# Kernel tuning notes

Hardware: AMD Instinct MI355X
Metric: run time of the kernel (lower is better)

## Reference

```python
import jax, jax.numpy as jnp
import numpy as np
from jax import lax

N_NODES = 10000
N_EDGES = 160000
F_NODE = 128
C_GCN = 64
S_SEQ = 32
T_SEQ = 96
H_LSTM = 128


def setup_inputs() -> dict:
    key = jax.random.key(0)
    ks = jax.random.split(key, 20)
    inp = {
        "sequences": jax.random.normal(ks[0], (N_NODES, T_SEQ, S_SEQ), jnp.float32),
        "edge_index": jax.random.randint(ks[1], (2, N_EDGES), 0, N_NODES, jnp.int64),
        "edge_attr": jax.random.uniform(ks[2], (N_EDGES, 1), jnp.float32),
        "node_features": jax.random.normal(ks[3], (N_NODES, F_NODE), jnp.float32),
        "node_indices": jax.random.randint(ks[4], (N_NODES,), 0, N_NODES, jnp.int64),
    }
    s_g = 1.0 / np.sqrt(F_NODE)
    inp["gcn_w"] = jax.random.uniform(ks[5], (F_NODE, C_GCN), jnp.float32, -s_g, s_g)
    inp["gcn_b"] = jnp.zeros((C_GCN,), jnp.float32)
    in0 = S_SEQ + C_GCN
    s_l = 1.0 / np.sqrt(H_LSTM)
    inp["w_ih0"] = jax.random.uniform(ks[6], (4 * H_LSTM, in0), jnp.float32, -s_l, s_l)
    inp["w_hh0"] = jax.random.uniform(ks[7], (4 * H_LSTM, H_LSTM), jnp.float32, -s_l, s_l)
    inp["b_ih0"] = jax.random.uniform(ks[8], (4 * H_LSTM,), jnp.float32, -s_l, s_l)
    inp["b_hh0"] = jax.random.uniform(ks[9], (4 * H_LSTM,), jnp.float32, -s_l, s_l)
    inp["w_ih1"] = jax.random.uniform(ks[10], (4 * H_LSTM, H_LSTM), jnp.float32, -s_l, s_l)
    inp["w_hh1"] = jax.random.uniform(ks[11], (4 * H_LSTM, H_LSTM), jnp.float32, -s_l, s_l)
    inp["b_ih1"] = jax.random.uniform(ks[12], (4 * H_LSTM,), jnp.float32, -s_l, s_l)
    inp["b_hh1"] = jax.random.uniform(ks[13], (4 * H_LSTM,), jnp.float32, -s_l, s_l)
    s_f = 1.0 / np.sqrt(H_LSTM)
    inp["fc_w"] = jax.random.uniform(ks[14], (1, H_LSTM), jnp.float32, -s_f, s_f)
    inp["fc_b"] = jnp.zeros((1,), jnp.float32)
    return inp


def gcn_conv(x, edge_index, w, b):
    """PyG GCNConv: out = D^{-1/2} (A + I) D^{-1/2} X W + b."""
    n = x.shape[0]
    xw = x @ w  # [N, C]
    loop = jnp.arange(n, dtype=edge_index.dtype)
    row = jnp.concatenate([edge_index[0], loop])  # source j
    col = jnp.concatenate([edge_index[1], loop])  # target i
    deg = jax.ops.segment_sum(jnp.ones_like(col, dtype=xw.dtype), col, num_segments=n)
    dinv = jnp.where(deg > 0, lax.rsqrt(deg), 0.0)
    norm = dinv[row] * dinv[col]  # [E+N]
    msg = xw[row] * norm[:, None]  # gather + scale
    out = jax.ops.segment_sum(msg, col, num_segments=n)  # scatter-add
    return out + b


def lstm_layer(x, w_ih, w_hh, b_ih, b_hh):
    """batch_first LSTM layer; torch gate order i,f,g,o. x: [N,T,I] -> [N,T,H]."""
    n, t, _ = x.shape
    h_dim = w_hh.shape[1]
    xg = jnp.einsum("nti,gi->ntg", x, w_ih) + b_ih + b_hh  # [N,T,4H]

    def step(carry, xt):
        h, c = carry
        g = xt + h @ w_hh.T
        i, f, gg, o = jnp.split(g, 4, axis=-1)
        c = jax.nn.sigmoid(f) * c + jax.nn.sigmoid(i) * jnp.tanh(gg)
        h = jax.nn.sigmoid(o) * jnp.tanh(c)
        return (h, c), h

    h0 = jnp.zeros((n, h_dim), x.dtype)
    _, hs = lax.scan(step, (h0, h0), jnp.swapaxes(xg, 0, 1))
    return jnp.swapaxes(hs, 0, 1)


def reference(sequences, edge_index, edge_attr, node_features, node_indices,
              gcn_w, gcn_b, w_ih0, w_hh0, b_ih0, b_hh0,
              w_ih1, w_hh1, b_ih1, b_hh1, fc_w, fc_b):
    # GCN over the static graph (dropout = identity in eval mode)
    gcn_out = gcn_conv(node_features, edge_index, gcn_w, gcn_b)  # [N, C]
    t = sequences.shape[1]
    gcn_rep = jnp.broadcast_to(gcn_out[:, None, :], (gcn_out.shape[0], t, gcn_out.shape[1]))
    combined = jnp.concatenate([sequences, gcn_rep], axis=-1)  # [N, T, S+C]
    h = lstm_layer(combined, w_ih0, w_hh0, b_ih0, b_hh0)
    h = lstm_layer(h, w_ih1, w_hh1, b_ih1, b_hh1)
    last = h[:, -1, :]  # [N, H]
    return last @ fc_w.T + fc_b  # [N, 1]
```

## Files before the change

### kernel.cpp

```cpp
#include <hip/hip_runtime.h>
#include <hip/hip_bf16.h>

typedef _Float16 half8 __attribute__((ext_vector_type(8)));
typedef float floatx4 __attribute__((ext_vector_type(4)));
typedef float floatx2 __attribute__((ext_vector_type(2)));

#define N_NODES 10000
#define F_NODE  128
#define C_GCN   64
#define N_EDGES 160000
#define T_SEQ   96
#define S_SEQ   32
#define HID     128
#define M_BLK   40
#define MT      3
#define SEQ_STRIDE 104
#define H_STRIDE   136
#define WAVE_STREAM 61440

__device__ __forceinline__ float fast_rcp(float x) { return __builtin_amdgcn_rcpf(x); }
__device__ __forceinline__ float sigm_f(float x) {
    return fast_rcp(1.0f + __expf(-x));
}
__device__ __forceinline__ float tanh_f(float x) {
    return 2.0f * fast_rcp(1.0f + __expf(-2.0f * x)) - 1.0f;
}

__global__ void k_gcn_xw(const float* __restrict__ nf, const float* __restrict__ w,
                         float* __restrict__ xw) {
    int tid = blockIdx.x * 256 + threadIdx.x;
    int n = tid >> 6, c = tid & 63;
    if (n >= N_NODES) return;
    float s = 0.f;
    #pragma unroll 8
    for (int k = 0; k < F_NODE; ++k) s = fmaf(nf[n * F_NODE + k], w[k * C_GCN + c], s);
    xw[n * C_GCN + c] = s;
}

__global__ void k_deg_init(float* __restrict__ deg) {
    int i = blockIdx.x * 256 + threadIdx.x;
    if (i < N_NODES) deg[i] = 1.0f;
}

__global__ void k_deg_count(const int* __restrict__ ei, float* __restrict__ deg) {
    int e = blockIdx.x * 256 + threadIdx.x;
    if (e < N_EDGES) atomicAdd(&deg[ei[N_EDGES + e]], 1.0f);
}

__global__ void k_dinv(const float* __restrict__ deg, float* __restrict__ dinv) {
    int i = blockIdx.x * 256 + threadIdx.x;
    if (i < N_NODES) dinv[i] = rsqrtf(deg[i]);
}

__global__ void k_gcn_self(const float* __restrict__ xw, const float* __restrict__ dinv,
                           const float* __restrict__ gb, float* __restrict__ gout) {
    int tid = blockIdx.x * 256 + threadIdx.x;
    int n = tid >> 6, c = tid & 63;
    if (n >= N_NODES) return;
    float di = dinv[n];
    gout[tid] = xw[tid] * di * di + gb[c];
}

__global__ void k_gcn_scatter(const int* __restrict__ ei, const float* __restrict__ xw,
                              const float* __restrict__ dinv, float* __restrict__ gout) {
    int e = blockIdx.x * 4 + (threadIdx.x >> 6);
    int c = threadIdx.x & 63;
    if (e >= N_EDGES) return;
    int r  = ei[e];
    int cl = ei[N_EDGES + e];
    float nm = dinv[r] * dinv[cl];
    atomicAdd(&gout[cl * C_GCN + c], xw[r * C_GCN + c] * nm);
}

__global__ void k_pack(const float* __restrict__ w_ih0, const float* __restrict__ w_hh0,
                       const float* __restrict__ w_ih1, const float* __restrict__ w_hh1,
                       half8* __restrict__ pP) {
    int tid = blockIdx.x * 256 + threadIdx.x;
    if (tid >= 8 * 15 * 4 * 64) return;
    int lane = tid & 63;
    int g    = (tid >> 6) & 3;
    int s    = (tid >> 8) % 15;
    int w    = tid / 3840;
    const float* src; int kt, K;
    if (s < 3)       { src = w_ih0; kt = s;      K = 96;  }
    else if (s < 7)  { src = w_hh0; kt = s - 3;  K = 128; }
    else if (s < 11) { src = w_ih1; kt = s - 7;  K = 128; }
    else             { src = w_hh1; kt = s - 11; K = 128; }
    int row = g * 128 + w * 16 + (lane & 15);
    int k0  = kt * 32 + (lane >> 4) * 8;
    half8 v;
    #pragma unroll
    for (int j = 0; j < 8; ++j) v[j] = (_Float16)src[row * K + k0 + j];
    pP[tid] = v;
}

__global__ void k_bsum(const float* __restrict__ bi0, const float* __restrict__ bh0,
                       const float* __restrict__ bi1, const float* __restrict__ bh1,
                       float* __restrict__ bs) {
    int i = blockIdx.x * 256 + threadIdx.x;
    if (i < 512)       bs[i] = bi0[i] + bh0[i];
    else if (i < 1024) bs[i] = bi1[i - 512] + bh1[i - 512];
}


__device__ __forceinline__ void async_copy16(const void* g, void* l) {
    __builtin_amdgcn_global_load_lds(
        (const __attribute__((address_space(1))) unsigned int*)g,
        (__attribute__((address_space(3))) unsigned int*)l, 16, 0, 0);
}

__device__ __forceinline__ void dma_slot(const char* __restrict__ src, int lane, _Float16* slot) {
    #pragma unroll
    for (int g = 0; g < 4; ++g)
        async_copy16((const void*)(src + g * 1024 + lane * 16), (void*)(slot + g * 512));
}

#define VMW(N) asm volatile("s_waitcnt vmcnt(" #N ")" ::: "memory")

#define BARRIER_NOVM() do {                                   \
    asm volatile("s_waitcnt lgkmcnt(0)" ::: "memory");        \
    __builtin_amdgcn_s_barrier();                             \
    asm volatile("" ::: "memory");                            \
} while (0)

#define RDB(BG, BUF) {                                                      \
    _Pragma("unroll")                                                       \
    for (int g = 0; g < 4; ++g) (BG)[g] = *(const half8*)((BUF) + g * 512 + lane * 8); }

#define RDA(AA, APTR, KOFF, ASTR) {                                         \
    _Pragma("unroll")                                                       \
    for (int mt = 0; mt < MT; ++mt)                                         \
        (AA)[mt] = *(const half8*)((APTR) + (mt * 16 + l15) * (ASTR) + (KOFF) + quad * 8); }

#define MM(AA, BG) {                                                        \
    _Pragma("unroll")                                                       \
    for (int g = 0; g < 4; ++g)                                             \
        _Pragma("unroll")                                                   \
        for (int mt = 0; mt < MT; ++mt)                                     \
            acc[g][mt] = __builtin_amdgcn_mfma_f32_16x16x32_f16((AA)[mt], (BG)[g], acc[g][mt], 0, 0, 0); }

#define ACCINIT(B) {                                                        \
    _Pragma("unroll")                                                       \
    for (int g = 0; g < 4; ++g) {                                           \
        floatx4 bv = {(B)[g], (B)[g], (B)[g], (B)[g]};                      \
        _Pragma("unroll")                                                   \
        for (int mt = 0; mt < MT; ++mt) acc[g][mt] = bv;                    \
    } }

__device__ __forceinline__ void epilogue(floatx4 acc[4][MT],
                                         float c[MT][4], _Float16* Hnext,
                                         int quad, int ch) {
    #pragma unroll
    for (int mt = 0; mt < MT; ++mt) {
        #pragma unroll
        for (int r = 0; r < 4; ++r) {
            float gi = acc[0][mt][r];
            float gf = acc[1][mt][r];
            float gg = acc[2][mt][r];
            float go = acc[3][mt][r];
            float cn = sigm_f(gf) * c[mt][r] + sigm_f(gi) * tanh_f(gg);
            c[mt][r] = cn;
            float h = sigm_f(go) * tanh_f(cn);
            Hnext[(mt * 16 + quad * 4 + r) * H_STRIDE + ch] = (_Float16)h;
        }
    }
}

__global__ __launch_bounds__(512, 2) void k_lstm(
    const float* __restrict__ seq, const float* __restrict__ gcn,
    const char* __restrict__ pW, const float* __restrict__ bsum,
    const float* __restrict__ fcw, const float* __restrict__ fcb,
    float* __restrict__ out) {

    __shared__ __align__(16) _Float16 sSeq[48 * SEQ_STRIDE];
    __shared__ __align__(16) _Float16 sH0[2][48 * H_STRIDE];
    __shared__ __align__(16) _Float16 sH1[2][48 * H_STRIDE];
    __shared__ __align__(16) _Float16 sWa[8][2048];
    __shared__ __align__(16) _Float16 sWb[8][2048];
    __shared__ __align__(16) _Float16 sWc[8][2048];

    const int tid  = threadIdx.x;
    const int wid  = tid >> 6;
    const int lane = tid & 63;
    const int l15  = lane & 15;
    const int quad = lane >> 4;
    const int node0 = blockIdx.x * M_BLK;
    const int ch = wid * 16 + l15;
    const bool rot = (wid >= 4);

    _Float16* const rb0 = &sWa[wid][0];
    _Float16* const rb1 = &sWb[wid][0];
    _Float16* const rb2 = &sWc[wid][0];

    const char* pWw = pW + wid * WAVE_STREAM;

#define DMA(S, RB) dma_slot(pWw + (S) * 4096, lane, (RB))

    if (!rot) { DMA(0, rb0); DMA(1, rb1); }
    else      { DMA(3, rb0); DMA(4, rb1); }

    for (int i = tid; i < 48 * SEQ_STRIDE; i += 512) sSeq[i] = (_Float16)0.f;
    for (int i = tid; i < 48 * H_STRIDE; i += 512) {
        sH0[0][i] = (_Float16)0.f; sH0[1][i] = (_Float16)0.f;
        sH1[0][i] = (_Float16)0.f; sH1[1][i] = (_Float16)0.f;
    }

    float bias0[4], bias1[4];
    #pragma unroll
    for (int g = 0; g < 4; ++g) {
        bias0[g] = bsum[g * 128 + ch];
        bias1[g] = bsum[512 + g * 128 + ch];
    }

    float c0[MT][4] = {{0}}, c1[MT][4] = {{0}};

    __syncthreads();

    for (int i = tid; i < M_BLK * (C_GCN / 2); i += 512) {
        int r = i >> 5, cp = (i & 31) * 2;
        floatx2 v = *(const floatx2*)(gcn + (size_t)(node0 + r) * C_GCN + cp);
        sSeq[r * SEQ_STRIDE + S_SEQ + cp]     = (_Float16)v.x;
        sSeq[r * SEQ_STRIDE + S_SEQ + cp + 1] = (_Float16)v.y;
    }
    {
        int r = tid >> 4, cp = (tid & 15) * 2;
        if (tid < M_BLK * 16) {
            floatx2 v = *(const floatx2*)(seq + ((size_t)(node0 + r) * T_SEQ) * S_SEQ + cp);
            sSeq[r * SEQ_STRIDE + cp]     = (_Float16)v.x;
            sSeq[r * SEQ_STRIDE + cp + 1] = (_Float16)v.y;
        }
    }
    __syncthreads();

    floatx4 acc[4][MT];
    half8 aX[MT], aY[MT], bX[4], bY[4];

    RDB(bX, rb0);

    const int pr = tid >> 4, pc = (tid & 15) * 2;
    const int r1 = 32 + ((tid & 127) >> 4);
    floatx2 pfa, pfb;

    if (!rot) {
      for (int t = 0; t < T_SEQ; ++t) {
        const int cur = t & 1, nxt = cur ^ 1;
        const _Float16* h0c = &sH0[cur][0];
        _Float16*       h0n = &sH0[nxt][0];
        const _Float16* h1c = &sH1[cur][0];
        _Float16*       h1n = &sH1[nxt][0];
        {
            int tp = (t + 1 < T_SEQ) ? (t + 1) : (T_SEQ - 1);
            pfa = *(const floatx2*)(seq + ((size_t)(node0 + pr) * T_SEQ + tp) * S_SEQ + pc);
            pfb = *(const floatx2*)(seq + ((size_t)(node0 + r1) * T_SEQ + tp) * S_SEQ + pc);
        }
        ACCINIT(bias0);
        RDA(aX, sSeq, 0, SEQ_STRIDE);
        DMA(2, rb2);  VMW(6); RDB(bY, rb1); RDA(aY, sSeq, 32, SEQ_STRIDE); MM(aX, bX);
        DMA(3, rb0);  VMW(4); RDB(bX, rb2); RDA(aX, sSeq, 64, SEQ_STRIDE); MM(aY, bY);
        DMA(4, rb1);  VMW(4); RDB(bY, rb0); RDA(aY, h0c, 0,  H_STRIDE);    MM(aX, bX);
        DMA(5, rb2);  VMW(4); RDB(bX, rb1); RDA(aX, h0c, 32, H_STRIDE);    MM(aY, bY);
        DMA(6, rb0);  VMW(4); RDB(bY, rb2); RDA(aY, h0c, 64, H_STRIDE);    MM(aX, bX);
        DMA(7, rb1);  VMW(4); RDB(bX, rb0); RDA(aX, h0c, 96, H_STRIDE);    MM(aY, bY);
        DMA(8, rb2);  VMW(4); RDB(bY, rb1);                                MM(aX, bX);
        epilogue(acc, c0, h0n, quad, ch);
        BARRIER_NOVM();
        ACCINIT(bias1);
        RDA(aY, h0n, 0, H_STRIDE);
        DMA(9,  rb0); VMW(4); RDB(bX, rb2); RDA(aX, h0n, 32, H_STRIDE); MM(aY, bY);
        DMA(10, rb1); VMW(4); RDB(bY, rb0); RDA(aY, h0n, 64, H_STRIDE); MM(aX, bX);
        DMA(11, rb2); VMW(4); RDB(bX, rb1); RDA(aX, h0n, 96, H_STRIDE); MM(aY, bY);
        DMA(12, rb0); VMW(4); RDB(bY, rb2); RDA(aY, h1c, 0,  H_STRIDE); MM(aX, bX);
        DMA(13, rb1); VMW(4); RDB(bX, rb0); RDA(aX, h1c, 32, H_STRIDE); MM(aY, bY);
        DMA(14, rb2); VMW(4); RDB(bY, rb1); RDA(aY, h1c, 64, H_STRIDE); MM(aX, bX);
        DMA(0,  rb0); VMW(4); RDB(bX, rb2); RDA(aX, h1c, 96, H_STRIDE); MM(aY, bY);
        DMA(1,  rb1); VMW(4); MM(aX, bX);   RDB(bX, rb0);
        if (t + 1 < T_SEQ) {
            sSeq[pr * SEQ_STRIDE + pc]     = (_Float16)pfa.x;
            sSeq[pr * SEQ_STRIDE + pc + 1] = (_Float16)pfa.y;
            if (tid < 128) {
                sSeq[r1 * SEQ_STRIDE + pc]     = (_Float16)pfb.x;
                sSeq[r1 * SEQ_STRIDE + pc + 1] = (_Float16)pfb.y;
            }
        }
        epilogue(acc, c1, h1n, quad, ch);
        BARRIER_NOVM();
      }
    } else {
      for (int t = 0; t < T_SEQ; ++t) {
        const int cur = t & 1, nxt = cur ^ 1;
        const _Float16* h0c = &sH0[cur][0];
        _Float16*       h0n = &sH0[nxt][0];
        const _Float16* h1c = &sH1[cur][0];
        _Float16*       h1n = &sH1[nxt][0];
        {
            int tp = (t + 1 < T_SEQ) ? (t + 1) : (T_SEQ - 1);
            pfa = *(const floatx2*)(seq + ((size_t)(node0 + pr) * T_SEQ + tp) * S_SEQ + pc);
            pfb = *(const floatx2*)(seq + ((size_t)(node0 + r1) * T_SEQ + tp) * S_SEQ + pc);
        }
        ACCINIT(bias0);
        RDA(aX, h0c, 0, H_STRIDE);
        DMA(5,  rb2); VMW(6); RDB(bY, rb1); RDA(aY, h0c, 32, H_STRIDE);    MM(aX, bX);
        DMA(6,  rb0); VMW(4); RDB(bX, rb2); RDA(aX, h0c, 64, H_STRIDE);    MM(aY, bY);
        DMA(0,  rb1); VMW(4); RDB(bY, rb0); RDA(aY, h0c, 96, H_STRIDE);    MM(aX, bX);
        DMA(1,  rb2); VMW(4); RDB(bX, rb1); RDA(aX, sSeq, 0,  SEQ_STRIDE); MM(aY, bY);
        DMA(2,  rb0); VMW(4); RDB(bY, rb2); RDA(aY, sSeq, 32, SEQ_STRIDE); MM(aX, bX);
        DMA(11, rb1); VMW(4); RDB(bX, rb0); RDA(aX, sSeq, 64, SEQ_STRIDE); MM(aY, bY);
        DMA(12, rb2); VMW(4); RDB(bY, rb1);                                MM(aX, bX);
        epilogue(acc, c0, h0n, quad, ch);
        BARRIER_NOVM();
        ACCINIT(bias1);
        RDA(aY, h1c, 0, H_STRIDE);
        DMA(13, rb0); VMW(4); RDB(bX, rb2); RDA(aX, h1c, 32, H_STRIDE); MM(aY, bY);
        DMA(14, rb1); VMW(4); RDB(bY, rb0); RDA(aY, h1c, 64, H_STRIDE); MM(aX, bX);
        DMA(7,  rb2); VMW(4); RDB(bX, rb1); RDA(aX, h1c, 96, H_STRIDE); MM(aY, bY);
        DMA(8,  rb0); VMW(4); RDB(bY, rb2); RDA(aY, h0n, 0,  H_STRIDE); MM(aX, bX);
        DMA(9,  rb1); VMW(4); RDB(bX, rb0); RDA(aX, h0n, 32, H_STRIDE); MM(aY, bY);
        DMA(10, rb2); VMW(4); RDB(bY, rb1); RDA(aY, h0n, 64, H_STRIDE); MM(aX, bX);
        DMA(3,  rb0); VMW(4); RDB(bX, rb2); RDA(aX, h0n, 96, H_STRIDE); MM(aY, bY);
        DMA(4,  rb1); VMW(4); MM(aX, bX);   RDB(bX, rb0);
        if (t + 1 < T_SEQ) {
            sSeq[pr * SEQ_STRIDE + pc]     = (_Float16)pfa.x;
            sSeq[pr * SEQ_STRIDE + pc + 1] = (_Float16)pfa.y;
            if (tid < 128) {
                sSeq[r1 * SEQ_STRIDE + pc]     = (_Float16)pfb.x;
                sSeq[r1 * SEQ_STRIDE + pc + 1] = (_Float16)pfb.y;
            }
        }
        epilogue(acc, c1, h1n, quad, ch);
        BARRIER_NOVM();
      }
    }

#undef DMA

    asm volatile("s_waitcnt vmcnt(0)" ::: "memory");

    if (tid < M_BLK) {
        const _Float16* h1 = &sH1[0][tid * H_STRIDE];
        float s = fcb[0];
        #pragma unroll 16
        for (int k = 0; k < HID; ++k) s = fmaf((float)h1[k], fcw[k], s);
        out[node0 + tid] = s;
    }
}

extern "C" void kernel_launch(void* const* d_in, const int* in_sizes, int n_in,
                              void* d_out, int out_size, void* d_ws, size_t ws_size,
                              hipStream_t stream) {
    const float* seq   = (const float*)d_in[0];
    const int*   ei    = (const int*)d_in[1];
    const float* nf    = (const float*)d_in[3];
    const float* gcn_w = (const float*)d_in[5];
    const float* gcn_b = (const float*)d_in[6];
    const float* w_ih0 = (const float*)d_in[7];
    const float* w_hh0 = (const float*)d_in[8];
    const float* b_ih0 = (const float*)d_in[9];
    const float* b_hh0 = (const float*)d_in[10];
    const float* w_ih1 = (const float*)d_in[11];
    const float* w_hh1 = (const float*)d_in[12];
    const float* b_ih1 = (const float*)d_in[13];
    const float* b_hh1 = (const float*)d_in[14];
    const float* fc_w  = (const float*)d_in[15];
    const float* fc_b  = (const float*)d_in[16];
    float* out = (float*)d_out;

    char* ws = (char*)d_ws;
    float* xw   = (float*)(ws);
    float* gout = (float*)(ws + 2621440);
    float* deg  = (float*)(ws + 5242880);
    float* dinv = (float*)(ws + 5283840);
    float* bsum = (float*)(ws + 5324800);
    char*  pP   = (char*)(ws + 5328896);

    k_gcn_xw     <<<2500,  256, 0, stream>>>(nf, gcn_w, xw);
    k_deg_init   <<<40,    256, 0, stream>>>(deg);
    k_deg_count  <<<625,   256, 0, stream>>>(ei, deg);
    k_dinv       <<<40,    256, 0, stream>>>(deg, dinv);
    k_gcn_self   <<<2500,  256, 0, stream>>>(xw, dinv, gcn_b, gout);
    k_gcn_scatter<<<40000, 256, 0, stream>>>(ei, xw, dinv, gout);

    k_pack<<<120, 256, 0, stream>>>(w_ih0, w_hh0, w_ih1, w_hh1, (half8*)pP);
    k_bsum<<<4,   256, 0, stream>>>(b_ih0, b_hh0, b_ih1, b_hh1, bsum);

    k_lstm<<<250, 512, 0, stream>>>(seq, gout, pP, bsum, fc_w, fc_b, out);
}
```

Before: 1.161 ms.

## Keep six layer-0 weight k-tiles resident in registers, stream the rest

```diff
diff --git a/kernel.cpp b/kernel.cpp
--- a/kernel.cpp
+++ b/kernel.cpp
@@ -16,7 +16,9 @@
 #define MT      3
 #define SEQ_STRIDE 104
 #define H_STRIDE   136
-#define WAVE_STREAM 61440
+#define RES_SZ    196608
+#define RES_WAVE  24576
+#define STR_WAVE  36864
 
 __device__ __forceinline__ float fast_rcp(float x) { return __builtin_amdgcn_rcpf(x); }
 __device__ __forceinline__ float sigm_f(float x) {
@@ -74,24 +76,34 @@
 
 __global__ void k_pack(const float* __restrict__ w_ih0, const float* __restrict__ w_hh0,
                        const float* __restrict__ w_ih1, const float* __restrict__ w_hh1,
-                       half8* __restrict__ pP) {
+                       char* __restrict__ pP) {
     int tid = blockIdx.x * 256 + threadIdx.x;
-    if (tid >= 8 * 15 * 4 * 64) return;
+    if (tid >= 30720) return;
     int lane = tid & 63;
-    int g    = (tid >> 6) & 3;
-    int s    = (tid >> 8) % 15;
-    int w    = tid / 3840;
-    const float* src; int kt, K;
-    if (s < 3)       { src = w_ih0; kt = s;      K = 96;  }
-    else if (s < 7)  { src = w_hh0; kt = s - 3;  K = 128; }
-    else if (s < 11) { src = w_ih1; kt = s - 7;  K = 128; }
-    else             { src = w_hh1; kt = s - 11; K = 128; }
+    int rest = tid >> 6;
+    int w    = rest / 60;
+    int idx  = rest % 60;
+    const float* src; int K, kt, g;
+    size_t dst;
+    if (idx < 24) {
+        int i = idx >> 2; g = idx & 3;
+        int grp = i / 3; kt = i % 3;
+        src = grp ? w_hh0 : w_ih0; K = grp ? 128 : 96;
+        dst = (size_t)w * RES_WAVE + (size_t)idx * 1024 + lane * 16;
+    } else {
+        int j = idx - 24; int s = j >> 2; g = j & 3;
+        if (s == 0)      { src = w_hh0; kt = 3; }
+        else if (s <= 4) { src = w_ih1; kt = s - 1; }
+        else             { src = w_hh1; kt = s - 5; }
+        K = 128;
+        dst = (size_t)RES_SZ + (size_t)w * STR_WAVE + (size_t)s * 4096 + (size_t)g * 1024 + lane * 16;
+    }
     int row = g * 128 + w * 16 + (lane & 15);
     int k0  = kt * 32 + (lane >> 4) * 8;
     half8 v;
     #pragma unroll
     for (int j = 0; j < 8; ++j) v[j] = (_Float16)src[row * K + k0 + j];
-    pP[tid] = v;
+    *(half8*)(pP + dst) = v;
 }
 
 __global__ void k_bsum(const float* __restrict__ bi0, const float* __restrict__ bh0,
@@ -192,12 +204,19 @@
     _Float16* const rb1 = &sWb[wid][0];
     _Float16* const rb2 = &sWc[wid][0];
 
-    const char* pWw = pW + wid * WAVE_STREAM;
-
-#define DMA(S, RB) dma_slot(pWw + (S) * 4096, lane, (RB))
-
-    if (!rot) { DMA(0, rb0); DMA(1, rb1); }
-    else      { DMA(3, rb0); DMA(4, rb1); }
+    const char* pSw = pW + RES_SZ + (size_t)wid * STR_WAVE;
+
+#define DMA(S, RB) dma_slot(pSw + (S) * 4096, lane, (RB))
+
+    half8 rW[6][4];
+    {
+        const half8* pR = (const half8*)(pW + (size_t)wid * RES_WAVE);
+        #pragma unroll
+        for (int i = 0; i < 6; ++i)
+            #pragma unroll
+            for (int g = 0; g < 4; ++g)
+                rW[i][g] = pR[(i * 4 + g) * 64 + lane];
+    }
 
     for (int i = tid; i < 48 * SEQ_STRIDE; i += 512) sSeq[i] = (_Float16)0.f;
     for (int i = tid; i < 48 * H_STRIDE; i += 512) {
@@ -232,10 +251,11 @@
     }
     __syncthreads();
 
+    if (!rot) { DMA(0, rb0); DMA(1, rb1); DMA(2, rb2); }
+    else      { DMA(0, rb0); DMA(5, rb1); DMA(6, rb2); }
+
     floatx4 acc[4][MT];
     half8 aX[MT], aY[MT], bX[4], bY[4];
-
-    RDB(bX, rb0);
 
     const int pr = tid >> 4, pc = (tid & 15) * 2;
     const int r1 = 32 + ((tid & 127) >> 4);
@@ -255,25 +275,26 @@
         }
         ACCINIT(bias0);
         RDA(aX, sSeq, 0, SEQ_STRIDE);
-        DMA(2, rb2);  VMW(6); RDB(bY, rb1); RDA(aY, sSeq, 32, SEQ_STRIDE); MM(aX, bX);
-        DMA(3, rb0);  VMW(4); RDB(bX, rb2); RDA(aX, sSeq, 64, SEQ_STRIDE); MM(aY, bY);
-        DMA(4, rb1);  VMW(4); RDB(bY, rb0); RDA(aY, h0c, 0,  H_STRIDE);    MM(aX, bX);
-        DMA(5, rb2);  VMW(4); RDB(bX, rb1); RDA(aX, h0c, 32, H_STRIDE);    MM(aY, bY);
-        DMA(6, rb0);  VMW(4); RDB(bY, rb2); RDA(aY, h0c, 64, H_STRIDE);    MM(aX, bX);
-        DMA(7, rb1);  VMW(4); RDB(bX, rb0); RDA(aX, h0c, 96, H_STRIDE);    MM(aY, bY);
-        DMA(8, rb2);  VMW(4); RDB(bY, rb1);                                MM(aX, bX);
+        RDA(aY, sSeq, 32, SEQ_STRIDE);   MM(aX, rW[0]);
+        RDA(aX, sSeq, 64, SEQ_STRIDE);   MM(aY, rW[1]);
+        RDA(aY, h0c, 0,  H_STRIDE);      MM(aX, rW[2]);
+        RDA(aX, h0c, 32, H_STRIDE);      MM(aY, rW[3]);
+        RDA(aY, h0c, 64, H_STRIDE);      MM(aX, rW[4]);
+        VMW(8); RDB(bX, rb0);
+        RDA(aX, h0c, 96, H_STRIDE);      MM(aY, rW[5]);
+        MM(aX, bX);
         epilogue(acc, c0, h0n, quad, ch);
         BARRIER_NOVM();
         ACCINIT(bias1);
-        RDA(aY, h0n, 0, H_STRIDE);
-        DMA(9,  rb0); VMW(4); RDB(bX, rb2); RDA(aX, h0n, 32, H_STRIDE); MM(aY, bY);
-        DMA(10, rb1); VMW(4); RDB(bY, rb0); RDA(aY, h0n, 64, H_STRIDE); MM(aX, bX);
-        DMA(11, rb2); VMW(4); RDB(bX, rb1); RDA(aX, h0n, 96, H_STRIDE); MM(aY, bY);
-        DMA(12, rb0); VMW(4); RDB(bY, rb2); RDA(aY, h1c, 0,  H_STRIDE); MM(aX, bX);
-        DMA(13, rb1); VMW(4); RDB(bX, rb0); RDA(aX, h1c, 32, H_STRIDE); MM(aY, bY);
-        DMA(14, rb2); VMW(4); RDB(bY, rb1); RDA(aY, h1c, 64, H_STRIDE); MM(aX, bX);
-        DMA(0,  rb0); VMW(4); RDB(bX, rb2); RDA(aX, h1c, 96, H_STRIDE); MM(aY, bY);
-        DMA(1,  rb1); VMW(4); MM(aX, bX);   RDB(bX, rb0);
+        VMW(4); RDB(bY, rb1); RDA(aY, h0n, 0, H_STRIDE); DMA(3, rb0);
+        VMW(4); RDB(bX, rb2); RDA(aX, h0n, 32, H_STRIDE); MM(aY, bY); DMA(4, rb1);
+        VMW(4); RDB(bY, rb0); RDA(aY, h0n, 64, H_STRIDE); MM(aX, bX); DMA(5, rb2);
+        VMW(4); RDB(bX, rb1); RDA(aX, h0n, 96, H_STRIDE); MM(aY, bY); DMA(6, rb0);
+        VMW(4); RDB(bY, rb2); RDA(aY, h1c, 0,  H_STRIDE); MM(aX, bX); DMA(7, rb1);
+        VMW(4); RDB(bX, rb0); RDA(aX, h1c, 32, H_STRIDE); MM(aY, bY); DMA(8, rb2);
+        VMW(4); RDB(bY, rb1); RDA(aY, h1c, 64, H_STRIDE); MM(aX, bX); DMA(0, rb0);
+        VMW(4); RDB(bX, rb2); RDA(aX, h1c, 96, H_STRIDE); MM(aY, bY); DMA(1, rb1);
+        MM(aX, bX); DMA(2, rb2);
         if (t + 1 < T_SEQ) {
             sSeq[pr * SEQ_STRIDE + pc]     = (_Float16)pfa.x;
             sSeq[pr * SEQ_STRIDE + pc + 1] = (_Float16)pfa.y;
@@ -299,25 +320,26 @@
         }
         ACCINIT(bias0);
         RDA(aX, h0c, 0, H_STRIDE);
-        DMA(5,  rb2); VMW(6); RDB(bY, rb1); RDA(aY, h0c, 32, H_STRIDE);    MM(aX, bX);
-        DMA(6,  rb0); VMW(4); RDB(bX, rb2); RDA(aX, h0c, 64, H_STRIDE);    MM(aY, bY);
-        DMA(0,  rb1); VMW(4); RDB(bY, rb0); RDA(aY, h0c, 96, H_STRIDE);    MM(aX, bX);
-        DMA(1,  rb2); VMW(4); RDB(bX, rb1); RDA(aX, sSeq, 0,  SEQ_STRIDE); MM(aY, bY);
-        DMA(2,  rb0); VMW(4); RDB(bY, rb2); RDA(aY, sSeq, 32, SEQ_STRIDE); MM(aX, bX);
-        DMA(11, rb1); VMW(4); RDB(bX, rb0); RDA(aX, sSeq, 64, SEQ_STRIDE); MM(aY, bY);
-        DMA(12, rb2); VMW(4); RDB(bY, rb1);                                MM(aX, bX);
+        RDA(aY, h0c, 32, H_STRIDE);      MM(aX, rW[3]);
+        RDA(aX, h0c, 64, H_STRIDE);      MM(aY, rW[4]);
+        VMW(8); RDB(bX, rb0);
+        RDA(aY, h0c, 96, H_STRIDE);      MM(aX, rW[5]);
+        RDA(aX, sSeq, 0, SEQ_STRIDE);    MM(aY, bX);
+        RDA(aY, sSeq, 32, SEQ_STRIDE);   MM(aX, rW[0]);
+        RDA(aX, sSeq, 64, SEQ_STRIDE);   MM(aY, rW[1]);
+        MM(aX, rW[2]);
         epilogue(acc, c0, h0n, quad, ch);
         BARRIER_NOVM();
         ACCINIT(bias1);
-        RDA(aY, h1c, 0, H_STRIDE);
-        DMA(13, rb0); VMW(4); RDB(bX, rb2); RDA(aX, h1c, 32, H_STRIDE); MM(aY, bY);
-        DMA(14, rb1); VMW(4); RDB(bY, rb0); RDA(aY, h1c, 64, H_STRIDE); MM(aX, bX);
-        DMA(7,  rb2); VMW(4); RDB(bX, rb1); RDA(aX, h1c, 96, H_STRIDE); MM(aY, bY);
-        DMA(8,  rb0); VMW(4); RDB(bY, rb2); RDA(aY, h0n, 0,  H_STRIDE); MM(aX, bX);
-        DMA(9,  rb1); VMW(4); RDB(bX, rb0); RDA(aX, h0n, 32, H_STRIDE); MM(aY, bY);
-        DMA(10, rb2); VMW(4); RDB(bY, rb1); RDA(aY, h0n, 64, H_STRIDE); MM(aX, bX);
-        DMA(3,  rb0); VMW(4); RDB(bX, rb2); RDA(aX, h0n, 96, H_STRIDE); MM(aY, bY);
-        DMA(4,  rb1); VMW(4); MM(aX, bX);   RDB(bX, rb0);
+        VMW(4); RDB(bY, rb1); RDA(aY, h1c, 0, H_STRIDE); DMA(7, rb0);
+        VMW(4); RDB(bX, rb2); RDA(aX, h1c, 32, H_STRIDE); MM(aY, bY); DMA(8, rb1);
+        VMW(4); RDB(bY, rb0); RDA(aY, h1c, 64, H_STRIDE); MM(aX, bX); DMA(1, rb2);
+        VMW(4); RDB(bX, rb1); RDA(aX, h1c, 96, H_STRIDE); MM(aY, bY); DMA(2, rb0);
+        VMW(4); RDB(bY, rb2); RDA(aY, h0n, 0,  H_STRIDE); MM(aX, bX); DMA(3, rb1);
+        VMW(4); RDB(bX, rb0); RDA(aX, h0n, 32, H_STRIDE); MM(aY, bY); DMA(4, rb2);
+        VMW(4); RDB(bY, rb1); RDA(aY, h0n, 64, H_STRIDE); MM(aX, bX); DMA(0, rb0);
+        VMW(4); RDB(bX, rb2); RDA(aX, h0n, 96, H_STRIDE); MM(aY, bY); DMA(5, rb1);
+        MM(aX, bX); DMA(6, rb2);
         if (t + 1 < T_SEQ) {
             sSeq[pr * SEQ_STRIDE + pc]     = (_Float16)pfa.x;
             sSeq[pr * SEQ_STRIDE + pc + 1] = (_Float16)pfa.y;
@@ -379,7 +401,7 @@
     k_gcn_self   <<<2500,  256, 0, stream>>>(xw, dinv, gcn_b, gout);
     k_gcn_scatter<<<40000, 256, 0, stream>>>(ei, xw, dinv, gout);
 
-    k_pack<<<120, 256, 0, stream>>>(w_ih0, w_hh0, w_ih1, w_hh1, (half8*)pP);
+    k_pack<<<120, 256, 0, stream>>>(w_ih0, w_hh0, w_ih1, w_hh1, pP);
     k_bsum<<<4,   256, 0, stream>>>(b_ih0, b_hh0, b_ih1, b_hh1, bsum);
 
     k_lstm<<<250, 512, 0, stream>>>(seq, gout, pP, bsum, fc_w, fc_b, out);
```

Measured after the change: 1.967 ms. 1.69x slower.

## Defer layer-1 LSTM epilogue into next step's layer-0 MFMA sequence

Applied to the files above, without the earlier changes.

```diff
diff --git a/kernel.cpp b/kernel.cpp
--- a/kernel.cpp
+++ b/kernel.cpp
@@ -132,20 +132,42 @@
     for (int mt = 0; mt < MT; ++mt)                                         \
         (AA)[mt] = *(const half8*)((APTR) + (mt * 16 + l15) * (ASTR) + (KOFF) + quad * 8); }
 
-#define MM(AA, BG) {                                                        \
+#define MM(ACC, AA, BG) {                                                   \
     _Pragma("unroll")                                                       \
     for (int g = 0; g < 4; ++g)                                             \
         _Pragma("unroll")                                                   \
         for (int mt = 0; mt < MT; ++mt)                                     \
-            acc[g][mt] = __builtin_amdgcn_mfma_f32_16x16x32_f16((AA)[mt], (BG)[g], acc[g][mt], 0, 0, 0); }
-
-#define ACCINIT(B) {                                                        \
+            (ACC)[g][mt] = __builtin_amdgcn_mfma_f32_16x16x32_f16((AA)[mt], (BG)[g], (ACC)[g][mt], 0, 0, 0); }
+
+#define ACCINIT(ACC, B) {                                                   \
     _Pragma("unroll")                                                       \
     for (int g = 0; g < 4; ++g) {                                           \
         floatx4 bv = {(B)[g], (B)[g], (B)[g], (B)[g]};                      \
         _Pragma("unroll")                                                   \
-        for (int mt = 0; mt < MT; ++mt) acc[g][mt] = bv;                    \
+        for (int mt = 0; mt < MT; ++mt) (ACC)[g][mt] = bv;                  \
     } }
+
+#define EPIC(MT_) if (t) {                                                  \
+    _Pragma("unroll")                                                       \
+    for (int r = 0; r < 4; ++r) {                                           \
+        float gi = acc1[0][MT_][r];                                         \
+        float gf = acc1[1][MT_][r];                                         \
+        float gg = acc1[2][MT_][r];                                         \
+        float go = acc1[3][MT_][r];                                         \
+        float cn = sigm_f(gf) * c1[MT_][r] + sigm_f(gi) * tanh_f(gg);       \
+        c1[MT_][r] = cn;                                                    \
+        h1b[(MT_ * 16 + quad * 4 + r) * H_STRIDE + ch] = (_Float16)(sigm_f(go) * tanh_f(cn)); } }
+
+#define EPICT(MT_) {                                                        \
+    _Pragma("unroll")                                                       \
+    for (int r = 0; r < 4; ++r) {                                           \
+        float gi = acc1[0][MT_][r];                                         \
+        float gf = acc1[1][MT_][r];                                         \
+        float gg = acc1[2][MT_][r];                                         \
+        float go = acc1[3][MT_][r];                                         \
+        float cn = sigm_f(gf) * c1[MT_][r] + sigm_f(gi) * tanh_f(gg);       \
+        c1[MT_][r] = cn;                                                    \
+        h1b[(MT_ * 16 + quad * 4 + r) * H_STRIDE + ch] = (_Float16)(sigm_f(go) * tanh_f(cn)); } }
 
 __device__ __forceinline__ void epilogue(floatx4 acc[4][MT],
                                          float c[MT][4], _Float16* Hnext,
@@ -174,7 +196,7 @@
 
     __shared__ __align__(16) _Float16 sSeq[48 * SEQ_STRIDE];
     __shared__ __align__(16) _Float16 sH0[2][48 * H_STRIDE];
-    __shared__ __align__(16) _Float16 sH1[2][48 * H_STRIDE];
+    __shared__ __align__(16) _Float16 sH1[48 * H_STRIDE];
     __shared__ __align__(16) _Float16 sWa[8][2048];
     __shared__ __align__(16) _Float16 sWb[8][2048];
     __shared__ __align__(16) _Float16 sWc[8][2048];
@@ -191,6 +213,7 @@
     _Float16* const rb0 = &sWa[wid][0];
     _Float16* const rb1 = &sWb[wid][0];
     _Float16* const rb2 = &sWc[wid][0];
+    _Float16* const h1b = &sH1[0];
 
     const char* pWw = pW + wid * WAVE_STREAM;
 
@@ -202,7 +225,7 @@
     for (int i = tid; i < 48 * SEQ_STRIDE; i += 512) sSeq[i] = (_Float16)0.f;
     for (int i = tid; i < 48 * H_STRIDE; i += 512) {
         sH0[0][i] = (_Float16)0.f; sH0[1][i] = (_Float16)0.f;
-        sH1[0][i] = (_Float16)0.f; sH1[1][i] = (_Float16)0.f;
+        sH1[i] = (_Float16)0.f;
     }
 
     float bias0[4], bias1[4];
@@ -232,7 +255,7 @@
     }
     __syncthreads();
 
-    floatx4 acc[4][MT];
+    floatx4 acc0[4][MT], acc1[4][MT];
     half8 aX[MT], aY[MT], bX[4], bY[4];
 
     RDB(bX, rb0);
@@ -246,34 +269,32 @@
         const int cur = t & 1, nxt = cur ^ 1;
         const _Float16* h0c = &sH0[cur][0];
         _Float16*       h0n = &sH0[nxt][0];
-        const _Float16* h1c = &sH1[cur][0];
-        _Float16*       h1n = &sH1[nxt][0];
         {
             int tp = (t + 1 < T_SEQ) ? (t + 1) : (T_SEQ - 1);
             pfa = *(const floatx2*)(seq + ((size_t)(node0 + pr) * T_SEQ + tp) * S_SEQ + pc);
             pfb = *(const floatx2*)(seq + ((size_t)(node0 + r1) * T_SEQ + tp) * S_SEQ + pc);
         }
-        ACCINIT(bias0);
+        ACCINIT(acc0, bias0);
         RDA(aX, sSeq, 0, SEQ_STRIDE);
-        DMA(2, rb2);  VMW(6); RDB(bY, rb1); RDA(aY, sSeq, 32, SEQ_STRIDE); MM(aX, bX);
-        DMA(3, rb0);  VMW(4); RDB(bX, rb2); RDA(aX, sSeq, 64, SEQ_STRIDE); MM(aY, bY);
-        DMA(4, rb1);  VMW(4); RDB(bY, rb0); RDA(aY, h0c, 0,  H_STRIDE);    MM(aX, bX);
-        DMA(5, rb2);  VMW(4); RDB(bX, rb1); RDA(aX, h0c, 32, H_STRIDE);    MM(aY, bY);
-        DMA(6, rb0);  VMW(4); RDB(bY, rb2); RDA(aY, h0c, 64, H_STRIDE);    MM(aX, bX);
-        DMA(7, rb1);  VMW(4); RDB(bX, rb0); RDA(aX, h0c, 96, H_STRIDE);    MM(aY, bY);
-        DMA(8, rb2);  VMW(4); RDB(bY, rb1);                                MM(aX, bX);
-        epilogue(acc, c0, h0n, quad, ch);
+        DMA(2, rb2);  VMW(6); RDB(bY, rb1); RDA(aY, sSeq, 32, SEQ_STRIDE); MM(acc0, aX, bX);
+        DMA(3, rb0);  VMW(4); RDB(bX, rb2); RDA(aX, sSeq, 64, SEQ_STRIDE); MM(acc0, aY, bY); EPIC(0);
+        DMA(4, rb1);  VMW(4); RDB(bY, rb0); RDA(aY, h0c, 0,  H_STRIDE);    MM(acc0, aX, bX);
+        DMA(5, rb2);  VMW(4); RDB(bX, rb1); RDA(aX, h0c, 32, H_STRIDE);    MM(acc0, aY, bY); EPIC(1);
+        DMA(6, rb0);  VMW(4); RDB(bY, rb2); RDA(aY, h0c, 64, H_STRIDE);    MM(acc0, aX, bX);
+        DMA(7, rb1);  VMW(4); RDB(bX, rb0); RDA(aX, h0c, 96, H_STRIDE);    MM(acc0, aY, bY); EPIC(2);
+        DMA(8, rb2);  VMW(4); RDB(bY, rb1);                                MM(acc0, aX, bX);
+        epilogue(acc0, c0, h0n, quad, ch);
         BARRIER_NOVM();
-        ACCINIT(bias1);
+        ACCINIT(acc1, bias1);
         RDA(aY, h0n, 0, H_STRIDE);
-        DMA(9,  rb0); VMW(4); RDB(bX, rb2); RDA(aX, h0n, 32, H_STRIDE); MM(aY, bY);
-        DMA(10, rb1); VMW(4); RDB(bY, rb0); RDA(aY, h0n, 64, H_STRIDE); MM(aX, bX);
-        DMA(11, rb2); VMW(4); RDB(bX, rb1); RDA(aX, h0n, 96, H_STRIDE); MM(aY, bY);
-        DMA(12, rb0); VMW(4); RDB(bY, rb2); RDA(aY, h1c, 0,  H_STRIDE); MM(aX, bX);
-        DMA(13, rb1); VMW(4); RDB(bX, rb0); RDA(aX, h1c, 32, H_STRIDE); MM(aY, bY);
-        DMA(14, rb2); VMW(4); RDB(bY, rb1); RDA(aY, h1c, 64, H_STRIDE); MM(aX, bX);
-        DMA(0,  rb0); VMW(4); RDB(bX, rb2); RDA(aX, h1c, 96, H_STRIDE); MM(aY, bY);
-        DMA(1,  rb1); VMW(4); MM(aX, bX);   RDB(bX, rb0);
+        DMA(9,  rb0); VMW(4); RDB(bX, rb2); RDA(aX, h0n, 32, H_STRIDE); MM(acc1, aY, bY);
+        DMA(10, rb1); VMW(4); RDB(bY, rb0); RDA(aY, h0n, 64, H_STRIDE); MM(acc1, aX, bX);
+        DMA(11, rb2); VMW(4); RDB(bX, rb1); RDA(aX, h0n, 96, H_STRIDE); MM(acc1, aY, bY);
+        DMA(12, rb0); VMW(4); RDB(bY, rb2); RDA(aY, h1b, 0,  H_STRIDE); MM(acc1, aX, bX);
+        DMA(13, rb1); VMW(4); RDB(bX, rb0); RDA(aX, h1b, 32, H_STRIDE); MM(acc1, aY, bY);
+        DMA(14, rb2); VMW(4); RDB(bY, rb1); RDA(aY, h1b, 64, H_STRIDE); MM(acc1, aX, bX);
+        DMA(0,  rb0); VMW(4); RDB(bX, rb2); RDA(aX, h1b, 96, H_STRIDE); MM(acc1, aY, bY);
+        DMA(1,  rb1); VMW(4); MM(acc1, aX, bX);   RDB(bX, rb0);
         if (t + 1 < T_SEQ) {
             sSeq[pr * SEQ_STRIDE + pc]     = (_Float16)pfa.x;
             sSeq[pr * SEQ_STRIDE + pc + 1] = (_Float16)pfa.y;
@@ -282,7 +303,6 @@
                 sSeq[r1 * SEQ_STRIDE + pc + 1] = (_Float16)pfb.y;
             }
         }
-        epilogue(acc, c1, h1n, quad, ch);
         BARRIER_NOVM();
       }
     } else {
@@ -290,34 +310,32 @@
         const int cur = t & 1, nxt = cur ^ 1;
         const _Float16* h0c = &sH0[cur][0];
         _Float16*       h0n = &sH0[nxt][0];
-        const _Float16* h1c = &sH1[cur][0];
-        _Float16*       h1n = &sH1[nxt][0];
         {
             int tp = (t + 1 < T_SEQ) ? (t + 1) : (T_SEQ - 1);
             pfa = *(const floatx2*)(seq + ((size_t)(node0 + pr) * T_SEQ + tp) * S_SEQ + pc);
             pfb = *(const floatx2*)(seq + ((size_t)(node0 + r1) * T_SEQ + tp) * S_SEQ + pc);
         }
-        ACCINIT(bias0);
+        ACCINIT(acc0, bias0);
         RDA(aX, h0c, 0, H_STRIDE);
-        DMA(5,  rb2); VMW(6); RDB(bY, rb1); RDA(aY, h0c, 32, H_STRIDE);    MM(aX, bX);
-        DMA(6,  rb0); VMW(4); RDB(bX, rb2); RDA(aX, h0c, 64, H_STRIDE);    MM(aY, bY);
-        DMA(0,  rb1); VMW(4); RDB(bY, rb0); RDA(aY, h0c, 96, H_STRIDE);    MM(aX, bX);
-        DMA(1,  rb2); VMW(4); RDB(bX, rb1); RDA(aX, sSeq, 0,  SEQ_STRIDE); MM(aY, bY);
-        DMA(2,  rb0); VMW(4); RDB(bY, rb2); RDA(aY, sSeq, 32, SEQ_STRIDE); MM(aX, bX);
-        DMA(11, rb1); VMW(4); RDB(bX, rb0); RDA(aX, sSeq, 64, SEQ_STRIDE); MM(aY, bY);
-        DMA(12, rb2); VMW(4); RDB(bY, rb1);                                MM(aX, bX);
-        epilogue(acc, c0, h0n, quad, ch);
+        DMA(5,  rb2); VMW(6); RDB(bY, rb1); RDA(aY, h0c, 32, H_STRIDE);    MM(acc0, aX, bX);
+        DMA(6,  rb0); VMW(4); RDB(bX, rb2); RDA(aX, h0c, 64, H_STRIDE);    MM(acc0, aY, bY); EPIC(0);
+        DMA(0,  rb1); VMW(4); RDB(bY, rb0); RDA(aY, h0c, 96, H_STRIDE);    MM(acc0, aX, bX);
+        DMA(1,  rb2); VMW(4); RDB(bX, rb1); RDA(aX, sSeq, 0,  SEQ_STRIDE); MM(acc0, aY, bY); EPIC(1);
+        DMA(2,  rb0); VMW(4); RDB(bY, rb2); RDA(aY, sSeq, 32, SEQ_STRIDE); MM(acc0, aX, bX);
+        DMA(11, rb1); VMW(4); RDB(bX, rb0); RDA(aX, sSeq, 64, SEQ_STRIDE); MM(acc0, aY, bY); EPIC(2);
+        DMA(12, rb2); VMW(4); RDB(bY, rb1);                                MM(acc0, aX, bX);
+        epilogue(acc0, c0, h0n, quad, ch);
         BARRIER_NOVM();
-        ACCINIT(bias1);
-        RDA(aY, h1c, 0, H_STRIDE);
-        DMA(13, rb0); VMW(4); RDB(bX, rb2); RDA(aX, h1c, 32, H_STRIDE); MM(aY, bY);
-        DMA(14, rb1); VMW(4); RDB(bY, rb0); RDA(aY, h1c, 64, H_STRIDE); MM(aX, bX);
-        DMA(7,  rb2); VMW(4); RDB(bX, rb1); RDA(aX, h1c, 96, H_STRIDE); MM(aY, bY);
-        DMA(8,  rb0); VMW(4); RDB(bY, rb2); RDA(aY, h0n, 0,  H_STRIDE); MM(aX, bX);
-        DMA(9,  rb1); VMW(4); RDB(bX, rb0); RDA(aX, h0n, 32, H_STRIDE); MM(aY, bY);
-        DMA(10, rb2); VMW(4); RDB(bY, rb1); RDA(aY, h0n, 64, H_STRIDE); MM(aX, bX);
-        DMA(3,  rb0); VMW(4); RDB(bX, rb2); RDA(aX, h0n, 96, H_STRIDE); MM(aY, bY);
-        DMA(4,  rb1); VMW(4); MM(aX, bX);   RDB(bX, rb0);
+        ACCINIT(acc1, bias1);
+        RDA(aY, h1b, 0, H_STRIDE);
+        DMA(13, rb0); VMW(4); RDB(bX, rb2); RDA(aX, h1b, 32, H_STRIDE); MM(acc1, aY, bY);
+        DMA(14, rb1); VMW(4); RDB(bY, rb0); RDA(aY, h1b, 64, H_STRIDE); MM(acc1, aX, bX);
+        DMA(7,  rb2); VMW(4); RDB(bX, rb1); RDA(aX, h1b, 96, H_STRIDE); MM(acc1, aY, bY);
+        DMA(8,  rb0); VMW(4); RDB(bY, rb2); RDA(aY, h0n, 0,  H_STRIDE); MM(acc1, aX, bX);
+        DMA(9,  rb1); VMW(4); RDB(bX, rb0); RDA(aX, h0n, 32, H_STRIDE); MM(acc1, aY, bY);
+        DMA(10, rb2); VMW(4); RDB(bY, rb1); RDA(aY, h0n, 64, H_STRIDE); MM(acc1, aX, bX);
+        DMA(3,  rb0); VMW(4); RDB(bX, rb2); RDA(aX, h0n, 96, H_STRIDE); MM(acc1, aY, bY);
+        DMA(4,  rb1); VMW(4); MM(acc1, aX, bX);   RDB(bX, rb0);
         if (t + 1 < T_SEQ) {
             sSeq[pr * SEQ_STRIDE + pc]     = (_Float16)pfa.x;
             sSeq[pr * SEQ_STRIDE + pc + 1] = (_Float16)pfa.y;
@@ -326,17 +344,18 @@
                 sSeq[r1 * SEQ_STRIDE + pc + 1] = (_Float16)pfb.y;
             }
         }
-        epilogue(acc, c1, h1n, quad, ch);
         BARRIER_NOVM();
       }
     }
 
 #undef DMA
 
+    EPICT(0); EPICT(1); EPICT(2);
     asm volatile("s_waitcnt vmcnt(0)" ::: "memory");
+    __syncthreads();
 
     if (tid < M_BLK) {
-        const _Float16* h1 = &sH1[0][tid * H_STRIDE];
+        const _Float16* h1 = &sH1[tid * H_STRIDE];
         float s = fcb[0];
         #pragma unroll 16
         for (int k = 0; k < HID; ++k) s = fmaf((float)h1[k], fcw[k], s);
```

Result: slower. 2.049 ms (+76.4%).

## Double-buffer sequence tile and drop one barrier per LSTM timestep

Applied to the files above, without the earlier changes.

```diff
diff --git a/kernel.cpp b/kernel.cpp
--- a/kernel.cpp
+++ b/kernel.cpp
@@ -14,7 +14,8 @@
 #define HID     128
 #define M_BLK   40
 #define MT      3
-#define SEQ_STRIDE 104
+#define SEQ_STRIDE 32
+#define GCN_STRIDE 72
 #define H_STRIDE   136
 #define WAVE_STREAM 61440
 
@@ -147,6 +148,14 @@
         for (int mt = 0; mt < MT; ++mt) acc[g][mt] = bv;                    \
     } }
 
+#define COMMIT_SEQ() do { if (t + 1 < T_SEQ) {                              \
+        seqW[pr * SEQ_STRIDE + pc]     = (_Float16)pfa.x;                   \
+        seqW[pr * SEQ_STRIDE + pc + 1] = (_Float16)pfa.y;                   \
+        if (tid < 128) {                                                    \
+            seqW[r1 * SEQ_STRIDE + pc]     = (_Float16)pfb.x;               \
+            seqW[r1 * SEQ_STRIDE + pc + 1] = (_Float16)pfb.y;               \
+        } } } while (0)
+
 __device__ __forceinline__ void epilogue(floatx4 acc[4][MT],
                                          float c[MT][4], _Float16* Hnext,
                                          int quad, int ch) {
@@ -172,7 +181,8 @@
     const float* __restrict__ fcw, const float* __restrict__ fcb,
     float* __restrict__ out) {
 
-    __shared__ __align__(16) _Float16 sSeq[48 * SEQ_STRIDE];
+    __shared__ __align__(16) _Float16 sSeqA[2][48 * SEQ_STRIDE];
+    __shared__ __align__(16) _Float16 sGcn[48 * GCN_STRIDE];
     __shared__ __align__(16) _Float16 sH0[2][48 * H_STRIDE];
     __shared__ __align__(16) _Float16 sH1[2][48 * H_STRIDE];
     __shared__ __align__(16) _Float16 sWa[8][2048];
@@ -199,7 +209,10 @@
     if (!rot) { DMA(0, rb0); DMA(1, rb1); }
     else      { DMA(3, rb0); DMA(4, rb1); }
 
-    for (int i = tid; i < 48 * SEQ_STRIDE; i += 512) sSeq[i] = (_Float16)0.f;
+    for (int i = tid; i < 48 * SEQ_STRIDE; i += 512) {
+        sSeqA[0][i] = (_Float16)0.f; sSeqA[1][i] = (_Float16)0.f;
+    }
+    for (int i = tid; i < 48 * GCN_STRIDE; i += 512) sGcn[i] = (_Float16)0.f;
     for (int i = tid; i < 48 * H_STRIDE; i += 512) {
         sH0[0][i] = (_Float16)0.f; sH0[1][i] = (_Float16)0.f;
         sH1[0][i] = (_Float16)0.f; sH1[1][i] = (_Float16)0.f;
@@ -219,15 +232,15 @@
     for (int i = tid; i < M_BLK * (C_GCN / 2); i += 512) {
         int r = i >> 5, cp = (i & 31) * 2;
         floatx2 v = *(const floatx2*)(gcn + (size_t)(node0 + r) * C_GCN + cp);
-        sSeq[r * SEQ_STRIDE + S_SEQ + cp]     = (_Float16)v.x;
-        sSeq[r * SEQ_STRIDE + S_SEQ + cp + 1] = (_Float16)v.y;
+        sGcn[r * GCN_STRIDE + cp]     = (_Float16)v.x;
+        sGcn[r * GCN_STRIDE + cp + 1] = (_Float16)v.y;
     }
     {
         int r = tid >> 4, cp = (tid & 15) * 2;
         if (tid < M_BLK * 16) {
             floatx2 v = *(const floatx2*)(seq + ((size_t)(node0 + r) * T_SEQ) * S_SEQ + cp);
-            sSeq[r * SEQ_STRIDE + cp]     = (_Float16)v.x;
-            sSeq[r * SEQ_STRIDE + cp + 1] = (_Float16)v.y;
+            sSeqA[0][r * SEQ_STRIDE + cp]     = (_Float16)v.x;
+            sSeqA[0][r * SEQ_STRIDE + cp + 1] = (_Float16)v.y;
         }
     }
     __syncthreads();
@@ -244,25 +257,28 @@
     if (!rot) {
       for (int t = 0; t < T_SEQ; ++t) {
         const int cur = t & 1, nxt = cur ^ 1;
-        const _Float16* h0c = &sH0[cur][0];
-        _Float16*       h0n = &sH0[nxt][0];
-        const _Float16* h1c = &sH1[cur][0];
-        _Float16*       h1n = &sH1[nxt][0];
+        const _Float16* seqR = &sSeqA[cur][0];
+        _Float16*       seqW = &sSeqA[nxt][0];
+        const _Float16* h0c  = &sH0[cur][0];
+        _Float16*       h0n  = &sH0[nxt][0];
+        const _Float16* h1c  = &sH1[cur][0];
+        _Float16*       h1n  = &sH1[nxt][0];
         {
             int tp = (t + 1 < T_SEQ) ? (t + 1) : (T_SEQ - 1);
             pfa = *(const floatx2*)(seq + ((size_t)(node0 + pr) * T_SEQ + tp) * S_SEQ + pc);
             pfb = *(const floatx2*)(seq + ((size_t)(node0 + r1) * T_SEQ + tp) * S_SEQ + pc);
         }
         ACCINIT(bias0);
-        RDA(aX, sSeq, 0, SEQ_STRIDE);
-        DMA(2, rb2);  VMW(6); RDB(bY, rb1); RDA(aY, sSeq, 32, SEQ_STRIDE); MM(aX, bX);
-        DMA(3, rb0);  VMW(4); RDB(bX, rb2); RDA(aX, sSeq, 64, SEQ_STRIDE); MM(aY, bY);
+        RDA(aX, seqR, 0, SEQ_STRIDE);
+        DMA(2, rb2);  VMW(6); RDB(bY, rb1); RDA(aY, sGcn, 0,  GCN_STRIDE); MM(aX, bX);
+        DMA(3, rb0);  VMW(4); RDB(bX, rb2); RDA(aX, sGcn, 32, GCN_STRIDE); MM(aY, bY);
         DMA(4, rb1);  VMW(4); RDB(bY, rb0); RDA(aY, h0c, 0,  H_STRIDE);    MM(aX, bX);
         DMA(5, rb2);  VMW(4); RDB(bX, rb1); RDA(aX, h0c, 32, H_STRIDE);    MM(aY, bY);
         DMA(6, rb0);  VMW(4); RDB(bY, rb2); RDA(aY, h0c, 64, H_STRIDE);    MM(aX, bX);
         DMA(7, rb1);  VMW(4); RDB(bX, rb0); RDA(aX, h0c, 96, H_STRIDE);    MM(aY, bY);
         DMA(8, rb2);  VMW(4); RDB(bY, rb1);                                MM(aX, bX);
         epilogue(acc, c0, h0n, quad, ch);
+        COMMIT_SEQ();
         BARRIER_NOVM();
         ACCINIT(bias1);
         RDA(aY, h0n, 0, H_STRIDE);
@@ -274,24 +290,17 @@
         DMA(14, rb2); VMW(4); RDB(bY, rb1); RDA(aY, h1c, 64, H_STRIDE); MM(aX, bX);
         DMA(0,  rb0); VMW(4); RDB(bX, rb2); RDA(aX, h1c, 96, H_STRIDE); MM(aY, bY);
         DMA(1,  rb1); VMW(4); MM(aX, bX);   RDB(bX, rb0);
-        if (t + 1 < T_SEQ) {
-            sSeq[pr * SEQ_STRIDE + pc]     = (_Float16)pfa.x;
-            sSeq[pr * SEQ_STRIDE + pc + 1] = (_Float16)pfa.y;
-            if (tid < 128) {
-                sSeq[r1 * SEQ_STRIDE + pc]     = (_Float16)pfb.x;
-                sSeq[r1 * SEQ_STRIDE + pc + 1] = (_Float16)pfb.y;
-            }
-        }
         epilogue(acc, c1, h1n, quad, ch);
-        BARRIER_NOVM();
       }
     } else {
       for (int t = 0; t < T_SEQ; ++t) {
         const int cur = t & 1, nxt = cur ^ 1;
-        const _Float16* h0c = &sH0[cur][0];
-        _Float16*       h0n = &sH0[nxt][0];
-        const _Float16* h1c = &sH1[cur][0];
-        _Float16*       h1n = &sH1[nxt][0];
+        const _Float16* seqR = &sSeqA[cur][0];
+        _Float16*       seqW = &sSeqA[nxt][0];
+        const _Float16* h0c  = &sH0[cur][0];
+        _Float16*       h0n  = &sH0[nxt][0];
+        const _Float16* h1c  = &sH1[cur][0];
+        _Float16*       h1n  = &sH1[nxt][0];
         {
             int tp = (t + 1 < T_SEQ) ? (t + 1) : (T_SEQ - 1);
             pfa = *(const floatx2*)(seq + ((size_t)(node0 + pr) * T_SEQ + tp) * S_SEQ + pc);
@@ -299,14 +308,15 @@
         }
         ACCINIT(bias0);
         RDA(aX, h0c, 0, H_STRIDE);
-        DMA(5,  rb2); VMW(6); RDB(bY, rb1); RDA(aY, h0c, 32, H_STRIDE);    MM(aX, bX);
-        DMA(6,  rb0); VMW(4); RDB(bX, rb2); RDA(aX, h0c, 64, H_STRIDE);    MM(aY, bY);
-        DMA(0,  rb1); VMW(4); RDB(bY, rb0); RDA(aY, h0c, 96, H_STRIDE);    MM(aX, bX);
-        DMA(1,  rb2); VMW(4); RDB(bX, rb1); RDA(aX, sSeq, 0,  SEQ_STRIDE); MM(aY, bY);
-        DMA(2,  rb0); VMW(4); RDB(bY, rb2); RDA(aY, sSeq, 32, SEQ_STRIDE); MM(aX, bX);
-        DMA(11, rb1); VMW(4); RDB(bX, rb0); RDA(aX, sSeq, 64, SEQ_STRIDE); MM(aY, bY);
-        DMA(12, rb2); VMW(4); RDB(bY, rb1);                                MM(aX, bX);
+        DMA(5,  rb2); VMW(6); RDB(bY, rb1); RDA(aY, h0c, 32, H_STRIDE);     MM(aX, bX);
+        DMA(6,  rb0); VMW(4); RDB(bX, rb2); RDA(aX, h0c, 64, H_STRIDE);     MM(aY, bY);
+        DMA(0,  rb1); VMW(4); RDB(bY, rb0); RDA(aY, h0c, 96, H_STRIDE);     MM(aX, bX);
+        DMA(1,  rb2); VMW(4); RDB(bX, rb1); RDA(aX, seqR, 0, SEQ_STRIDE);   MM(aY, bY);
+        DMA(2,  rb0); VMW(4); RDB(bY, rb2); RDA(aY, sGcn, 0,  GCN_STRIDE);  MM(aX, bX);
+        DMA(11, rb1); VMW(4); RDB(bX, rb0); RDA(aX, sGcn, 32, GCN_STRIDE);  MM(aY, bY);
+        DMA(12, rb2); VMW(4); RDB(bY, rb1);                                 MM(aX, bX);
         epilogue(acc, c0, h0n, quad, ch);
+        COMMIT_SEQ();
         BARRIER_NOVM();
         ACCINIT(bias1);
         RDA(aY, h1c, 0, H_STRIDE);
@@ -318,22 +328,14 @@
         DMA(10, rb2); VMW(4); RDB(bY, rb1); RDA(aY, h0n, 64, H_STRIDE); MM(aX, bX);
         DMA(3,  rb0); VMW(4); RDB(bX, rb2); RDA(aX, h0n, 96, H_STRIDE); MM(aY, bY);
         DMA(4,  rb1); VMW(4); MM(aX, bX);   RDB(bX, rb0);
-        if (t + 1 < T_SEQ) {
-            sSeq[pr * SEQ_STRIDE + pc]     = (_Float16)pfa.x;
-            sSeq[pr * SEQ_STRIDE + pc + 1] = (_Float16)pfa.y;
-            if (tid < 128) {
-                sSeq[r1 * SEQ_STRIDE + pc]     = (_Float16)pfb.x;
-                sSeq[r1 * SEQ_STRIDE + pc + 1] = (_Float16)pfb.y;
-            }
-        }
         epilogue(acc, c1, h1n, quad, ch);
-        BARRIER_NOVM();
       }
     }
 
 #undef DMA
 
     asm volatile("s_waitcnt vmcnt(0)" ::: "memory");
+    __syncthreads();
 
     if (tid < M_BLK) {
         const _Float16* h1 = &sH1[0][tid * H_STRIDE];
```

Measured after the change: 1.756 ms. 1.51x slower.
